# Performance work log

Measured on AMD Instinct MI355X. Metric: run time of the kernel, lower is better.

The kernel has to match this reference:

```python
import jax, jax.numpy as jnp
import numpy as np

T, B, A, H = 1024, 16, 8, 256


def setup_inputs() -> dict:
    key = jax.random.key(0)
    ks = jax.random.split(key, 8)
    s = 1.0 / np.sqrt(H)  # approximate lecun/orthogonal scale for stability
    return {
        "ins": jax.random.normal(ks[0], (T, B, A, H), dtype=jnp.float32),
        "resets": jax.random.randint(ks[1], (T, B, A), 0, 2) == 1,
        "h0": jnp.zeros((B, A, H), dtype=jnp.float32),
        "W_ir": jax.random.normal(ks[2], (H, H), dtype=jnp.float32) * s,
        "W_iz": jax.random.normal(ks[3], (H, H), dtype=jnp.float32) * s,
        "W_in": jax.random.normal(ks[4], (H, H), dtype=jnp.float32) * s,
        "b_ir": jnp.zeros((H,), dtype=jnp.float32),
        "b_iz": jnp.zeros((H,), dtype=jnp.float32),
        "b_in": jnp.zeros((H,), dtype=jnp.float32),
        "W_hr": jax.random.normal(ks[5], (H, H), dtype=jnp.float32) * s,
        "W_hz": jax.random.normal(ks[6], (H, H), dtype=jnp.float32) * s,
        "W_hn": jax.random.normal(ks[7], (H, H), dtype=jnp.float32) * s,
        "b_hn": jnp.zeros((H,), dtype=jnp.float32),
    }


def reference(ins, resets, h0, W_ir, W_iz, W_in, b_ir, b_iz, b_in, W_hr, W_hz, W_hn, b_hn):
    # Precompute the input-side gate projections for all timesteps at once
    # (mathematically identical to flax GRUCell's per-step dense_i calls).
    xr = ins @ W_ir + b_ir  # [T, B, A, H]
    xz = ins @ W_iz + b_iz
    xn = ins @ W_in + b_in

    def step(h, xs):
        xr_t, xz_t, xn_t, rst_t = xs
        # reset masking: re-init carry to zeros where episode resets
        h = jnp.where(rst_t[..., None], jnp.zeros_like(h), h)
        r = jax.nn.sigmoid(xr_t + h @ W_hr)
        z = jax.nn.sigmoid(xz_t + h @ W_hz)
        n = jnp.tanh(xn_t + r * (h @ W_hn + b_hn))
        new_h = (1.0 - z) * n + z * h
        return new_h, new_h

    final_h, ys = jax.lax.scan(step, h0, (xr, xz, xn, resets))
    return ys  # [T, B, A, H]; final carry == ys[-1]
```

## Files before the change

### kernel.cpp

```cpp
#include <hip/hip_runtime.h>

#define BA 128
#define H 256
#define TH 768
#define NROWS (1024 * BA)
#define LCAP 65536
#define NBUCK 8
#define MT 32
#define AP 264
#define NFRAG (8 * 48 * 64)

typedef _Float16 h2_t __attribute__((ext_vector_type(2)));
typedef _Float16 h8_t __attribute__((ext_vector_type(8)));
typedef short s8_t __attribute__((ext_vector_type(8)));
typedef float f4_t __attribute__((ext_vector_type(4)));
typedef unsigned short u16;
typedef u16 us4_t __attribute__((ext_vector_type(4)));
typedef unsigned int u32;
typedef u32 v64u __attribute__((ext_vector_type(64)));

__device__ __forceinline__ float bf2f(u16 u) {
  union { u32 i; float f; } c; c.i = ((u32)u) << 16; return c.f;
}
__device__ __forceinline__ u16 f2bf(float f) {
  union { float f; u32 i; } c; c.f = f;
  u32 r = c.i + 0x7FFFu + ((c.i >> 16) & 1u);
  return (u16)(r >> 16);
}
__device__ __forceinline__ float sigm(float x) {
  float e = __builtin_amdgcn_exp2f(-x * 1.442695040888963f);
  return __builtin_amdgcn_rcpf(1.0f + e);
}
__device__ __forceinline__ float tanh_(float x) {
  float e = __builtin_amdgcn_exp2f(x * 2.885390081777927f);
  return 1.0f - 2.0f * __builtin_amdgcn_rcpf(1.0f + e);
}
__device__ __forceinline__ float ldf(const void* p, bool f32, size_t idx) {
  return f32 ? ((const float*)p)[idx] : bf2f(((const u16*)p)[idx]);
}
__device__ __forceinline__ int ldrst(const void* p, bool isbyte, size_t idx) {
  return isbyte ? (int)((const unsigned char*)p)[idx] : ((const int*)p)[idx];
}
__device__ __forceinline__ float F2(h2_t a, h2_t b, float c) {
#if defined(__has_builtin) && __has_builtin(__builtin_amdgcn_fdot2)
  return __builtin_amdgcn_fdot2(a, b, c, false);
#else
  return c + (float)a[0] * (float)b[0] + (float)a[1] * (float)b[1];
#endif
}

__global__ __launch_bounds__(256) void kdetect(const u32* __restrict__ insw,
                                               const u32* __restrict__ rstw,
                                               const u32* __restrict__ whrw,
                                               const u32* __restrict__ wirw,
                                               int* __restrict__ flags,
                                               int* __restrict__ cnt) {
  __shared__ int c0, c1, c2, c3;
  if (threadIdx.x == 0) { c0 = 0; c1 = 0; c2 = 0; c3 = 0; }
  if (threadIdx.x < NBUCK) cnt[threadIdx.x] = 0;
  __syncthreads();
  if (!(fabsf(bf2f((u16)(insw[threadIdx.x] & 0xFFFFu))) < 1e10f)) atomicAdd(&c0, 1);
  if (!(fabsf(bf2f((u16)(whrw[threadIdx.x] & 0xFFFFu))) < 1e10f)) atomicAdd(&c2, 1);
  if (!(fabsf(bf2f((u16)(wirw[threadIdx.x] & 0xFFFFu))) < 1e10f)) atomicAdd(&c3, 1);
  if (threadIdx.x < 128 && rstw[threadIdx.x] > 1u) atomicAdd(&c1, 1);
  __syncthreads();
  if (threadIdx.x == 0) {
    flags[0] = (c0 > 8) ? 1 : 0;
    flags[1] = (c1 > 0) ? 1 : 0;
    flags[2] = (c2 > 8) ? 1 : 0;
    flags[3] = (c3 > 8) ? 1 : 0;
  }
}

__global__ __launch_bounds__(256) void ktrans(const void* __restrict__ W0, const void* __restrict__ W1,
                                              const void* __restrict__ W2, const void* __restrict__ W3,
                                              const void* __restrict__ W4, const void* __restrict__ W5,
                                              u16* __restrict__ WT, const int* __restrict__ flags) {
  __shared__ u16 tile[64][65];
  int g = blockIdx.z;
  bool f32in = ((g < 3) ? flags[3] : flags[2]) != 0;
  bool toF16 = (g >= 3);
  const void* srcs[6] = {W0, W1, W2, W3, W4, W5};
  const void* src = srcs[g];
  int k0 = blockIdx.x * 64, j0 = blockIdx.y * 64;
  int tid = threadIdx.x;
#pragma unroll
  for (int p = 0; p < 16; ++p) {
    int e = p * 256 + tid;
    int kr = e >> 6, jc = e & 63;
    size_t idx = (size_t)(k0 + kr) * H + j0 + jc;
    float v = f32in ? ((const float*)src)[idx] : bf2f(((const u16*)src)[idx]);
    u16 bits;
    if (toF16) {
      _Float16 h = (_Float16)v;
      bits = __builtin_bit_cast(u16, h);
    } else {
      bits = f2bf(v);
    }
    tile[kr][jc] = bits;
  }
  __syncthreads();
  u16* dst = WT + (size_t)g * H * H;
#pragma unroll
  for (int p = 0; p < 16; ++p) {
    int e = p * 256 + tid;
    int jr = e >> 6, kc = e & 63;
    dst[(size_t)(j0 + jr) * H + k0 + kc] = tile[kc][jr];
  }
}

__global__ __launch_bounds__(256) void kswz(const u16* __restrict__ WT, u16* __restrict__ WB) {
  int fl = blockIdx.x * 256 + threadIdx.x;
  if (fl >= NFRAG) return;
  int part = blockIdx.y;
  int lane = fl & 63;
  int cg = (fl >> 6) % 48;
  int kk = (fl >> 6) / 48;
  int g = part * 3 + (cg >> 4);
  int col = ((cg & 15) << 4) + (lane & 15);
  int k0 = kk * 32 + ((lane >> 4) << 3);
  const u16* src = WT + (size_t)g * H * H + (size_t)col * H + k0;
  *(s8_t*)(WB + ((size_t)part * NFRAG + fl) * 8) = *(const s8_t*)src;
}

__global__ __launch_bounds__(256) void kgemm(const void* __restrict__ ins,
                                             int t0, const u16* __restrict__ WiB,
                                             u16* __restrict__ C,
                                             const int* __restrict__ flags) {
  __shared__ __align__(16) u16 As[64 * AP];
  bool f32in = flags[0] != 0;
  int tid = threadIdx.x;
  int bt = blockIdx.x;
  int rh = blockIdx.y;
  size_t abase = ((size_t)(t0 + bt) * BA + rh * 64) * H;
#pragma unroll
  for (int q = 0; q < 8; ++q) {
    int idx = q * 256 + tid;
    int row = idx >> 5;
    int col0 = (idx & 31) * 8;
    s8_t v;
    if (f32in) {
      const float* s = (const float*)ins + abase + (size_t)idx * 8;
      f4_t x0 = *(const f4_t*)s;
      f4_t x1 = *(const f4_t*)(s + 4);
#pragma unroll
      for (int i = 0; i < 4; ++i) v[i] = (short)f2bf(x0[i]);
#pragma unroll
      for (int i = 0; i < 4; ++i) v[4 + i] = (short)f2bf(x1[i]);
    } else {
      v = *(const s8_t*)((const u16*)ins + abase + (size_t)idx * 8);
    }
    *(s8_t*)(As + row * AP + col0) = v;
  }
  __syncthreads();

  int lane = tid & 63;
  int wv = tid >> 6;
  int wr = wv >> 1;
  int wc = wv & 1;
  int r16 = lane & 15;
  int kg = lane >> 4;
  const s8_t* WB = (const s8_t*)WiB;
  int row0 = bt * 128 + rh * 64;

  for (int c = 0; c < 6; ++c) {
    f4_t acc[2][4];
#pragma unroll
    for (int a = 0; a < 2; ++a)
#pragma unroll
      for (int b = 0; b < 4; ++b) acc[a][b] = (f4_t)0.0f;
#pragma unroll 2
    for (int kk = 0; kk < 8; ++kk) {
      s8_t af[2];
#pragma unroll
      for (int mt = 0; mt < 2; ++mt)
        af[mt] = *(const s8_t*)(As + (wr * 32 + mt * 16 + r16) * AP + kk * 32 + kg * 8);
      s8_t bfr[4];
#pragma unroll
      for (int ct = 0; ct < 4; ++ct) {
        int cg = c * 8 + wc * 4 + ct;
        bfr[ct] = WB[(size_t)((kk * 48 + cg) * 64 + lane)];
      }
#pragma unroll
      for (int ct = 0; ct < 4; ++ct)
#pragma unroll
        for (int mt = 0; mt < 2; ++mt)
          acc[mt][ct] = __builtin_amdgcn_mfma_f32_16x16x32_bf16(af[mt], bfr[ct], acc[mt][ct], 0, 0, 0);
    }
#pragma unroll
    for (int mt = 0; mt < 2; ++mt)
#pragma unroll
      for (int ct = 0; ct < 4; ++ct)
#pragma unroll
        for (int r = 0; r < 4; ++r) {
          int grow = row0 + wr * 32 + mt * 16 + kg * 4 + r;
          int gcol = c * 128 + wc * 64 + ct * 16 + r16;
          C[(size_t)grow * TH + gcol] = f2bf(acc[mt][ct][r]);
        }
  }
}

__global__ __launch_bounds__(256) void kdlists(const void* __restrict__ resets,
                                               unsigned char* __restrict__ dbuf,
                                               int* __restrict__ cnt,
                                               u32* __restrict__ list,
                                               const int* __restrict__ flags) {
  bool rbyte = flags[1] != 0;
  int w = blockIdx.x;
  int tid = threadIdx.x;
  __shared__ unsigned char rst[1024];
  __shared__ unsigned char dS[1024];
  __shared__ int lcnt[NBUCK], lbase[NBUCK], lpos[NBUCK];
  if (tid < NBUCK) { lcnt[tid] = 0; lpos[tid] = 0; }
  for (int t = tid; t < 1024; t += 256)
    rst[t] = (unsigned char)(ldrst(resets, rbyte, (size_t)t * BA + w) != 0);
  __syncthreads();
#pragma unroll
  for (int p = 0; p < 4; ++p) {
    int t = p * 256 + tid;
    int d;
    if (rst[t]) {
      d = 255;
    } else {
      int tr = t - 1;
      while (tr >= 0 && !rst[tr]) --tr;
      d = t - ((tr >= 0) ? tr : 0);
      if (d > 254) d = 254;
    }
    dS[t] = (unsigned char)d;
    if (d < NBUCK) atomicAdd(&lcnt[d], 1);
  }
  __syncthreads();
  if (tid < NBUCK) lbase[tid] = atomicAdd(&cnt[tid], lcnt[tid]);
  for (int t = tid; t < 1024; t += 256) dbuf[(size_t)w * 1024 + t] = dS[t];
  __syncthreads();
#pragma unroll
  for (int p = 0; p < 4; ++p) {
    int t = p * 256 + tid;
    int d = dS[t];
    if (d < NBUCK) {
      int pos = lbase[d] + atomicAdd(&lpos[d], 1);
      if (pos < LCAP) list[(size_t)d * LCAP + pos] = (u32)(t * BA + w);
    }
  }
}

__global__ __launch_bounds__(256) void kelem(const u16* __restrict__ xproj,
                                             const void* __restrict__ resets,
                                             float* __restrict__ out,
                                             const void* __restrict__ bir, const void* __restrict__ biz,
                                             const void* __restrict__ bin_, const void* __restrict__ bhn,
                                             const int* __restrict__ flags) {
  bool rbyte = flags[1] != 0;
  bool wf32 = flags[2] != 0;
  int j = threadIdx.x;
  float vbir = ldf(bir, wf32, j), vbiz = ldf(biz, wf32, j);
  float vbin = ldf(bin_, wf32, j), vbhn = ldf(bhn, wf32, j);
  for (int i = blockIdx.x; i < NROWS; i += gridDim.x) {
    if (!ldrst(resets, rbyte, i)) continue;
    size_t xb = (size_t)i * TH + j;
    float r = sigm(bf2f(xproj[xb]) + vbir);
    float z = sigm(bf2f(xproj[xb + H]) + vbiz);
    float n = tanh_(bf2f(xproj[xb + 2 * H]) + vbin + r * vbhn);
    out[(size_t)i * H + j] = (1.0f - z) * n;
  }
}

__global__ __launch_bounds__(512) void kstep(const u16* __restrict__ xproj,
                                             float* __restrict__ out,
                                             const void* __restrict__ h0,
                                             const u16* __restrict__ WhB,
                                             const int* __restrict__ cnt,
                                             const u32* __restrict__ list,
                                             const void* __restrict__ bir, const void* __restrict__ biz,
                                             const void* __restrict__ bin_, const void* __restrict__ bhn,
                                             const int* __restrict__ flags, int s) {
  int cs = cnt[s];
  if (cs <= 0) return;
  bool wf32 = flags[2] != 0;
  __shared__ __align__(16) u16 As[MT * AP];
  __shared__ int ridS[MT];
  int tid = threadIdx.x;
  int lane = tid & 63;
  int wv = tid >> 6;
  int r16 = lane & 15;
  int kg = lane >> 4;
  int ntiles = (cs + MT - 1) / MT;
  float vb[2][4];
#pragma unroll
  for (int jt = 0; jt < 2; ++jt) {
    int j = wv * 32 + jt * 16 + r16;
    vb[jt][0] = ldf(bir, wf32, j);
    vb[jt][1] = ldf(biz, wf32, j);
    vb[jt][2] = ldf(bin_, wf32, j);
    vb[jt][3] = ldf(bhn, wf32, j);
  }
  const s8_t* WB = (const s8_t*)WhB;

  for (int tile = blockIdx.x; tile < ntiles; tile += gridDim.x) {
    __syncthreads();
    {
      int i = tid >> 4;
      int seg = tid & 15;
      int idx = tile * MT + i;
      int rid = (idx < cs) ? (int)list[idx] : -1;
      if (seg == 0) ridS[i] = rid;
      u16* dst = As + i * AP + seg * 16;
      if (rid >= 0) {
        if (s == 0) {
#pragma unroll
          for (int q = 0; q < 4; ++q) {
            us4_t hb;
#pragma unroll
            for (int e = 0; e < 4; ++e) {
              _Float16 hh = (_Float16)ldf(h0, wf32, (size_t)rid * H + seg * 16 + q * 4 + e);
              hb[e] = __builtin_bit_cast(u16, hh);
            }
            *(us4_t*)(dst + q * 4) = hb;
          }
        } else {
          const float* src = out + (size_t)(rid - BA) * H + seg * 16;
#pragma unroll
          for (int q = 0; q < 4; ++q) {
            f4_t v = *(const f4_t*)(src + q * 4);
            us4_t hb;
#pragma unroll
            for (int e = 0; e < 4; ++e) {
              _Float16 hh = (_Float16)v[e];
              hb[e] = __builtin_bit_cast(u16, hh);
            }
            *(us4_t*)(dst + q * 4) = hb;
          }
        }
      } else {
        us4_t hz; hz[0] = 0; hz[1] = 0; hz[2] = 0; hz[3] = 0;
#pragma unroll
        for (int q = 0; q < 4; ++q) *(us4_t*)(dst + q * 4) = hz;
      }
    }
    __syncthreads();

    f4_t acc[2][6];
#pragma unroll
    for (int a = 0; a < 2; ++a)
#pragma unroll
      for (int b = 0; b < 6; ++b) acc[a][b] = (f4_t)0.0f;

#pragma unroll 2
    for (int kk = 0; kk < 8; ++kk) {
      h8_t af[2];
#pragma unroll
      for (int mt = 0; mt < 2; ++mt)
        af[mt] = __builtin_bit_cast(h8_t,
            *(const s8_t*)(As + (mt * 16 + r16) * AP + kk * 32 + kg * 8));
      s8_t bfr[6];
#pragma unroll
      for (int g = 0; g < 3; ++g)
#pragma unroll
        for (int jt = 0; jt < 2; ++jt) {
          int cg = g * 16 + wv * 2 + jt;
          bfr[g * 2 + jt] = WB[(size_t)((kk * 48 + cg) * 64 + lane)];
        }
#pragma unroll
      for (int c = 0; c < 6; ++c)
#pragma unroll
        for (int mt = 0; mt < 2; ++mt)
          acc[mt][c] = __builtin_amdgcn_mfma_f32_16x16x32_f16(
              af[mt], __builtin_bit_cast(h8_t, bfr[c]), acc[mt][c], 0, 0, 0);
    }

#pragma unroll
    for (int mt = 0; mt < 2; ++mt)
#pragma unroll
      for (int r = 0; r < 4; ++r) {
        int rowl = mt * 16 + kg * 4 + r;
        int rid = ridS[rowl];
        if (rid < 0) continue;
#pragma unroll
        for (int jt = 0; jt < 2; ++jt) {
          int j = wv * 32 + jt * 16 + r16;
          size_t xb = (size_t)rid * TH + j;
          float rg = sigm(bf2f(xproj[xb]) + vb[jt][0] + acc[mt][jt][r]);
          float zg = sigm(bf2f(xproj[xb + H]) + vb[jt][1] + acc[mt][2 + jt][r]);
          float ng = tanh_(bf2f(xproj[xb + 2 * H]) + vb[jt][2] + rg * (acc[mt][4 + jt][r] + vb[jt][3]));
          float hp = (s == 0) ? ldf(h0, wf32, (size_t)rid * H + j)
                              : out[(size_t)(rid - BA) * H + j];
          out[(size_t)rid * H + j] = (1.0f - zg) * ng + zg * hp;
        }
      }
  }
}

#define LDW(VR, P, c) { uint4 q_ = *(const uint4*)((P) + (c) * 8); \
  VR[(c)*4+0] = q_.x; VR[(c)*4+1] = q_.y; VR[(c)*4+2] = q_.z; VR[(c)*4+3] = q_.w; }
#define LDWALL(VR, P) \
  LDW(VR,P,0) LDW(VR,P,1) LDW(VR,P,2) LDW(VR,P,3) LDW(VR,P,4) LDW(VR,P,5) LDW(VR,P,6) LDW(VR,P,7) \
  LDW(VR,P,8) LDW(VR,P,9) LDW(VR,P,10) LDW(VR,P,11) LDW(VR,P,12) LDW(VR,P,13) LDW(VR,P,14) LDW(VR,P,15)

#define BCH(x) __builtin_bit_cast(h2_t, (u32)(x))
#define DOTC(c) { uint4 hv_ = h4_[c]; \
  h2_t a0_ = __builtin_bit_cast(h2_t, hv_.x); \
  h2_t a1_ = __builtin_bit_cast(h2_t, hv_.y); \
  h2_t a2_ = __builtin_bit_cast(h2_t, hv_.z); \
  h2_t a3_ = __builtin_bit_cast(h2_t, hv_.w); \
  ar = F2(BCH(WR[4*(c)+0]), a0_, ar); az = F2(BCH(WZ[4*(c)+0]), a0_, az); an = F2(BCH(WN[4*(c)+0]), a0_, an); \
  ar = F2(BCH(WR[4*(c)+1]), a1_, ar); az = F2(BCH(WZ[4*(c)+1]), a1_, az); an = F2(BCH(WN[4*(c)+1]), a1_, an); \
  ar = F2(BCH(WR[4*(c)+2]), a2_, ar); az = F2(BCH(WZ[4*(c)+2]), a2_, az); an = F2(BCH(WN[4*(c)+2]), a2_, an); \
  ar = F2(BCH(WR[4*(c)+3]), a3_, ar); az = F2(BCH(WZ[4*(c)+3]), a3_, az); an = F2(BCH(WN[4*(c)+3]), a3_, an); }
#define DOT16 \
  DOTC(0) DOTC(1) DOTC(2) DOTC(3) DOTC(4) DOTC(5) DOTC(6) DOTC(7) \
  DOTC(8) DOTC(9) DOTC(10) DOTC(11) DOTC(12) DOTC(13) DOTC(14) DOTC(15)

__global__ __launch_bounds__(512, 2) void ktail(const u16* __restrict__ xproj,
                                                float* __restrict__ out,
                                                const u16* __restrict__ WhF,
                                                const unsigned char* __restrict__ dbuf,
                                                const void* __restrict__ bir, const void* __restrict__ biz,
                                                const void* __restrict__ bin_, const void* __restrict__ bhn,
                                                const int* __restrict__ flags) {
  int w = blockIdx.x;
  int tid = threadIdx.x;
  int j = tid >> 1;
  int half = tid & 1;
  bool wf32 = flags[2] != 0;
  __shared__ __align__(16) u16 hsb[256];
  __shared__ unsigned char dcol[1024];
  for (int t = tid; t < 1024; t += 512) dcol[t] = dbuf[(size_t)w * 1024 + t];
  const u16* pr = WhF + (size_t)j * H + half * 128;
  const u16* pz = WhF + (size_t)H * H + (size_t)j * H + half * 128;
  const u16* pn = WhF + (size_t)2 * H * H + (size_t)j * H + half * 128;
  v64u WR, WZ, WN;
  LDWALL(WR, pr)
  LDWALL(WZ, pz)
  LDWALL(WN, pn)
  float vbir = ldf(bir, wf32, j), vbiz = ldf(biz, wf32, j);
  float vbin = ldf(bin_, wf32, j), vbhn = ldf(bhn, wf32, j);
  __syncthreads();
  int prev_t = -99;
  float hreg = 0.0f;
#pragma unroll 1
  for (int t = 0; t < 1024; ++t) {
    int d = dcol[t];
    if (d < NBUCK || d == 255) continue;
    if (prev_t != t - 1) {
      hreg = out[((size_t)(t - 1) * BA + w) * H + j];
      if (half == 0) { _Float16 hh = (_Float16)hreg; hsb[j] = __builtin_bit_cast(u16, hh); }
      __syncthreads();
    }
    const uint4* h4_ = (const uint4*)(&hsb[half * 128]);
    float ar = 0.0f, az = 0.0f, an = 0.0f;
    DOT16
    ar += __shfl_xor(ar, 1, 64);
    az += __shfl_xor(az, 1, 64);
    an += __shfl_xor(an, 1, 64);
    size_t xb = ((size_t)t * BA + w) * TH + j;
    float r = sigm(bf2f(xproj[xb]) + vbir + ar);
    float z = sigm(bf2f(xproj[xb + H]) + vbiz + az);
    float n = tanh_(bf2f(xproj[xb + 2 * H]) + vbin + r * (an + vbhn));
    float hnew = (1.0f - z) * n + z * hreg;
    if (half == 0) out[((size_t)t * BA + w) * H + j] = hnew;
    __syncthreads();
    if (half == 0) { _Float16 hh = (_Float16)hnew; hsb[j] = __builtin_bit_cast(u16, hh); }
    hreg = hnew;
    prev_t = t;
    __syncthreads();
  }
}

__global__ __launch_bounds__(512, 2) void kscan(
    const u16* __restrict__ xproj, const void* __restrict__ resets,
    const void* __restrict__ h0, float* __restrict__ carry,
    const u16* __restrict__ WhF,
    const void* __restrict__ bir, const void* __restrict__ biz, const void* __restrict__ bin_,
    const void* __restrict__ bhn, float* __restrict__ out, int t0, int Tc,
    const int* __restrict__ flags) {
  int w = blockIdx.x;
  int tid = threadIdx.x;
  int j = tid >> 1;
  int half = tid & 1;
  bool wf32 = flags[2] != 0;
  bool rbyte = flags[1] != 0;
  __shared__ __align__(16) u16 hsb[2][256];
  __shared__ int rstS[1024];

  for (int t = tid; t < Tc; t += 512)
    rstS[t] = ldrst(resets, rbyte, (size_t)(t0 + t) * BA + w);

  const u16* pr = WhF + (size_t)j * H + half * 128;
  const u16* pz = WhF + (size_t)H * H + (size_t)j * H + half * 128;
  const u16* pn = WhF + (size_t)2 * H * H + (size_t)j * H + half * 128;
  v64u WR, WZ, WN;
  LDWALL(WR, pr)
  LDWALL(WZ, pz)
  LDWALL(WN, pn)

  float vbir = ldf(bir, wf32, j), vbiz = ldf(biz, wf32, j);
  float vbin = ldf(bin_, wf32, j), vbhn = ldf(bhn, wf32, j);

  float hreg = (t0 == 0) ? ldf(h0, wf32, (size_t)w * H + j) : carry[(size_t)w * H + j];
  __syncthreads();
  if (rstS[0] != 0) hreg = 0.0f;
  if (half == 0) {
    _Float16 hh = (_Float16)hreg;
    hsb[0][j] = __builtin_bit_cast(u16, hh);
  }
  __syncthreads();

  size_t xb0 = (size_t)w * TH + j;
  u16 cxr = xproj[xb0], cxz = xproj[xb0 + H], cxn = xproj[xb0 + 2 * H];

#pragma unroll 1
  for (int tl = 0; tl < Tc; ++tl) {
    u16 nxr = 0, nxz = 0, nxn = 0;
    if (tl + 1 < Tc) {
      size_t nb = ((size_t)(tl + 1) * BA + w) * TH + j;
      nxr = xproj[nb]; nxz = xproj[nb + H]; nxn = xproj[nb + 2 * H];
    }
    const uint4* h4_ = (const uint4*)(&hsb[tl & 1][half * 128]);
    float ar = 0.0f, az = 0.0f, an = 0.0f;
    DOT16
    ar += __shfl_xor(ar, 1, 64);
    az += __shfl_xor(az, 1, 64);
    an += __shfl_xor(an, 1, 64);
    float r = sigm(bf2f(cxr) + vbir + ar);
    float z = sigm(bf2f(cxz) + vbiz + az);
    float n = tanh_(bf2f(cxn) + vbin + r * (an + vbhn));
    float hnew = (1.0f - z) * n + z * hreg;
    if (half == 0) out[((size_t)(t0 + tl) * BA + w) * H + j] = hnew;

    float hnext = hnew;
    if (tl + 1 < Tc && rstS[tl + 1] != 0) hnext = 0.0f;
    if (half == 0) {
      _Float16 hh = (_Float16)hnext;
      hsb[(tl & 1) ^ 1][j] = __builtin_bit_cast(u16, hh);
    }
    hreg = hnext;
    cxr = nxr; cxz = nxz; cxn = nxn;
    __syncthreads();
  }
  if (half == 0) carry[(size_t)w * H + j] = hreg;
}

extern "C" void kernel_launch(void* const* d_in, const int* in_sizes, int n_in,
                              void* d_out, int out_size, void* d_ws, size_t ws_size,
                              hipStream_t stream) {
  const void* ins = d_in[0];
  const void* resets = d_in[1];
  const void* h0 = d_in[2];
  const void* Wir = d_in[3];
  const void* Wiz = d_in[4];
  const void* Win = d_in[5];
  const void* bir = d_in[6];
  const void* biz = d_in[7];
  const void* bin_ = d_in[8];
  const void* Whr = d_in[9];
  const void* Whz = d_in[10];
  const void* Whn = d_in[11];
  const void* bhn = d_in[12];
  float* out = (float*)d_out;

  const size_t off_wt = 256;
  const size_t wt_bytes = (size_t)6 * H * H * 2;
  const size_t off_carry = off_wt + wt_bytes;
  const size_t off_cnt = off_carry + (size_t)BA * H * 4;
  const size_t off_dbuf = off_cnt + 256;
  const size_t off_list = off_dbuf + NROWS;
  const size_t off_wb = off_list + (size_t)NBUCK * LCAP * 4;
  const size_t wb_bytes = (size_t)2 * TH * H * 2;
  const size_t off_xproj = off_wb + wb_bytes;
  const size_t chunk_bytes = (size_t)BA * TH * 2;

  int* flags = (int*)d_ws;
  u16* WT = (u16*)((char*)d_ws + off_wt);
  float* carry = (float*)((char*)d_ws + off_carry);
  int* cnt = (int*)((char*)d_ws + off_cnt);
  unsigned char* dbuf = (unsigned char*)((char*)d_ws + off_dbuf);
  u32* list = (u32*)((char*)d_ws + off_list);
  u16* WB = (u16*)((char*)d_ws + off_wb);
  u16* xproj = (u16*)((char*)d_ws + off_xproj);

  kdetect<<<1, 256, 0, stream>>>((const u32*)ins, (const u32*)resets,
                                 (const u32*)Whr, (const u32*)Wir, flags, cnt);
  ktrans<<<dim3(4, 4, 6), 256, 0, stream>>>(Wir, Wiz, Win, Whr, Whz, Whn, WT, flags);
  kswz<<<dim3(96, 2), 256, 0, stream>>>(WT, WB);

  const u16* WiB = WB;
  const u16* WhB = WB + (size_t)NFRAG * 8;
  const u16* WhT = WT + (size_t)3 * H * H;
  if (ws_size >= off_xproj + (size_t)1024 * chunk_bytes) {
    kdlists<<<128, 256, 0, stream>>>(resets, dbuf, cnt, list, flags);
    kgemm<<<dim3(1024, 2), 256, 0, stream>>>(ins, 0, WiB, xproj, flags);
    kelem<<<1024, 256, 0, stream>>>(xproj, resets, out, bir, biz, bin_, bhn, flags);
    for (int s = 0; s < NBUCK; ++s)
      kstep<<<1024, 512, 0, stream>>>(xproj, out, h0, WhB, cnt, list + (size_t)s * LCAP,
                                      bir, biz, bin_, bhn, flags, s);
    ktail<<<128, 512, 0, stream>>>(xproj, out, WhT, dbuf, bir, biz, bin_, bhn, flags);
  } else {
    int Tc = 1024;
    while (Tc > 1 && off_xproj + (size_t)Tc * chunk_bytes > ws_size) Tc >>= 1;
    int nchunks = 1024 / Tc;
    for (int c = 0; c < nchunks; ++c) {
      int t0 = c * Tc;
      kgemm<<<dim3(Tc, 2), 256, 0, stream>>>(ins, t0, WiB, xproj, flags);
      kscan<<<128, 512, 0, stream>>>(xproj, resets, h0, carry, WhT,
                                     bir, biz, bin_, bhn, out, t0, Tc, flags);
    }
  }
}
```

Before: 742.4 us.

## Fuse distance-list, reset-element and bucket step kernels into one cooperative kernel

Replaces the kdlists, kelem and eight kstep launches with a single cooperative kernel of 256 blocks. Grid-wide syncs separate the phases and the per-bucket steps, and each block strides over tiles instead of using a 1024-block grid. The goal is to remove launch overhead and the gaps between roughly ten small launches. The cost is lower parallelism per bucket and the overhead of grid barriers. If the cooperative launch fails, the code falls back to the old launch sequence.

Result: slower. 1.468 ms (+97.7%).

```diff
diff --git a/kernel.cpp b/kernel.cpp
--- a/kernel.cpp
+++ b/kernel.cpp
@@ -1,4 +1,5 @@
 #include <hip/hip_runtime.h>
+#include <hip/hip_cooperative_groups.h>
 
 #define BA 128
 #define H 256
@@ -9,6 +10,8 @@
 #define MT 32
 #define AP 264
 #define NFRAG (8 * 48 * 64)
+
+namespace cg = cooperative_groups;
 
 typedef _Float16 h2_t __attribute__((ext_vector_type(2)));
 typedef _Float16 h8_t __attribute__((ext_vector_type(8)));
@@ -197,6 +200,194 @@
           int gcol = c * 128 + wc * 64 + ct * 16 + r16;
           C[(size_t)grow * TH + gcol] = f2bf(acc[mt][ct][r]);
         }
+  }
+}
+
+__global__ __launch_bounds__(512) void kfused(
+    const u16* __restrict__ xproj, const void* __restrict__ resets,
+    const void* __restrict__ h0, const u16* __restrict__ WhB,
+    unsigned char* __restrict__ dbuf, int* __restrict__ cnt,
+    u32* __restrict__ list, float* __restrict__ out,
+    const void* __restrict__ bir, const void* __restrict__ biz,
+    const void* __restrict__ bin_, const void* __restrict__ bhn,
+    const int* __restrict__ flags) {
+  cg::grid_group gg = cg::this_grid();
+  __shared__ __align__(16) u16 As[MT * AP];
+  __shared__ int ridS[MT];
+  int tid = threadIdx.x;
+  int bid = blockIdx.x;
+  bool rbyte = flags[1] != 0;
+  bool wf32 = flags[2] != 0;
+
+  if (bid < 128) {
+    unsigned char* rstS = (unsigned char*)As;
+    unsigned char* dS = rstS + 1024;
+    int w = bid;
+    if (tid < NBUCK) { ridS[tid] = 0; ridS[16 + tid] = 0; }
+    for (int t = tid; t < 1024; t += 512)
+      rstS[t] = (unsigned char)(ldrst(resets, rbyte, (size_t)t * BA + w) != 0);
+    __syncthreads();
+#pragma unroll
+    for (int p = 0; p < 2; ++p) {
+      int t = p * 512 + tid;
+      int d;
+      if (rstS[t]) {
+        d = 255;
+      } else {
+        int tr = t - 1;
+        while (tr >= 0 && !rstS[tr]) --tr;
+        d = t - ((tr >= 0) ? tr : 0);
+        if (d > 254) d = 254;
+      }
+      dS[t] = (unsigned char)d;
+      if (d < NBUCK) atomicAdd(&ridS[d], 1);
+    }
+    __syncthreads();
+    if (tid < NBUCK) ridS[8 + tid] = atomicAdd(&cnt[tid], ridS[tid]);
+    for (int t = tid; t < 1024; t += 512) dbuf[(size_t)w * 1024 + t] = dS[t];
+    __syncthreads();
+#pragma unroll
+    for (int p = 0; p < 2; ++p) {
+      int t = p * 512 + tid;
+      int d = dS[t];
+      if (d < NBUCK) {
+        int pos = ridS[8 + d] + atomicAdd(&ridS[16 + d], 1);
+        if (pos < LCAP) list[(size_t)d * LCAP + pos] = (u32)(t * BA + w);
+      }
+    }
+  }
+  {
+    int j = tid & 255;
+    int rp = tid >> 8;
+    float vbir = ldf(bir, wf32, j), vbiz = ldf(biz, wf32, j);
+    float vbin = ldf(bin_, wf32, j), vbhn = ldf(bhn, wf32, j);
+    for (int i = bid * 2 + rp; i < NROWS; i += 512) {
+      if (!ldrst(resets, rbyte, i)) continue;
+      size_t xb = (size_t)i * TH + j;
+      float r = sigm(bf2f(xproj[xb]) + vbir);
+      float z = sigm(bf2f(xproj[xb + H]) + vbiz);
+      float n = tanh_(bf2f(xproj[xb + 2 * H]) + vbin + r * vbhn);
+      out[(size_t)i * H + j] = (1.0f - z) * n;
+    }
+  }
+  __threadfence();
+  gg.sync();
+
+  int lane = tid & 63;
+  int wv = tid >> 6;
+  int r16 = lane & 15;
+  int kg = lane >> 4;
+  float vb[2][4];
+#pragma unroll
+  for (int jt = 0; jt < 2; ++jt) {
+    int j = wv * 32 + jt * 16 + r16;
+    vb[jt][0] = ldf(bir, wf32, j);
+    vb[jt][1] = ldf(biz, wf32, j);
+    vb[jt][2] = ldf(bin_, wf32, j);
+    vb[jt][3] = ldf(bhn, wf32, j);
+  }
+  const s8_t* WB = (const s8_t*)WhB;
+
+  for (int s = 0; s < NBUCK; ++s) {
+    int cs = cnt[s];
+    const u32* lst = list + (size_t)s * LCAP;
+    if (cs > 0) {
+      int ntiles = (cs + MT - 1) / MT;
+      for (int tile = bid; tile < ntiles; tile += 256) {
+        __syncthreads();
+        {
+          int i = tid >> 4;
+          int seg = tid & 15;
+          int idx = tile * MT + i;
+          int rid = (idx < cs) ? (int)lst[idx] : -1;
+          if (seg == 0) ridS[i] = rid;
+          u16* dst = As + i * AP + seg * 16;
+          if (rid >= 0) {
+            if (s == 0) {
+#pragma unroll
+              for (int q = 0; q < 4; ++q) {
+                us4_t hb;
+#pragma unroll
+                for (int e = 0; e < 4; ++e) {
+                  _Float16 hh = (_Float16)ldf(h0, wf32, (size_t)rid * H + seg * 16 + q * 4 + e);
+                  hb[e] = __builtin_bit_cast(u16, hh);
+                }
+                *(us4_t*)(dst + q * 4) = hb;
+              }
+            } else {
+              const float* src = out + (size_t)(rid - BA) * H + seg * 16;
+#pragma unroll
+              for (int q = 0; q < 4; ++q) {
+                f4_t v = *(const f4_t*)(src + q * 4);
+                us4_t hb;
+#pragma unroll
+                for (int e = 0; e < 4; ++e) {
+                  _Float16 hh = (_Float16)v[e];
+                  hb[e] = __builtin_bit_cast(u16, hh);
+                }
+                *(us4_t*)(dst + q * 4) = hb;
+              }
+            }
+          } else {
+            us4_t hz; hz[0] = 0; hz[1] = 0; hz[2] = 0; hz[3] = 0;
+#pragma unroll
+            for (int q = 0; q < 4; ++q) *(us4_t*)(dst + q * 4) = hz;
+          }
+        }
+        __syncthreads();
+
+        f4_t acc[2][6];
+#pragma unroll
+        for (int a = 0; a < 2; ++a)
+#pragma unroll
+          for (int b = 0; b < 6; ++b) acc[a][b] = (f4_t)0.0f;
+
+#pragma unroll 2
+        for (int kk = 0; kk < 8; ++kk) {
+          h8_t af[2];
+#pragma unroll
+          for (int mt = 0; mt < 2; ++mt)
+            af[mt] = __builtin_bit_cast(h8_t,
+                *(const s8_t*)(As + (mt * 16 + r16) * AP + kk * 32 + kg * 8));
+          s8_t bfr[6];
+#pragma unroll
+          for (int g = 0; g < 3; ++g)
+#pragma unroll
+            for (int jt = 0; jt < 2; ++jt) {
+              int cgf = g * 16 + wv * 2 + jt;
+              bfr[g * 2 + jt] = WB[(size_t)((kk * 48 + cgf) * 64 + lane)];
+            }
+#pragma unroll
+          for (int c = 0; c < 6; ++c)
+#pragma unroll
+            for (int mt = 0; mt < 2; ++mt)
+              acc[mt][c] = __builtin_amdgcn_mfma_f32_16x16x32_f16(
+                  af[mt], __builtin_bit_cast(h8_t, bfr[c]), acc[mt][c], 0, 0, 0);
+        }
+
+#pragma unroll
+        for (int mt = 0; mt < 2; ++mt)
+#pragma unroll
+          for (int r = 0; r < 4; ++r) {
+            int rowl = mt * 16 + kg * 4 + r;
+            int rid = ridS[rowl];
+            if (rid < 0) continue;
+#pragma unroll
+            for (int jt = 0; jt < 2; ++jt) {
+              int j = wv * 32 + jt * 16 + r16;
+              size_t xb = (size_t)rid * TH + j;
+              float rg = sigm(bf2f(xproj[xb]) + vb[jt][0] + acc[mt][jt][r]);
+              float zg = sigm(bf2f(xproj[xb + H]) + vb[jt][1] + acc[mt][2 + jt][r]);
+              float ng = tanh_(bf2f(xproj[xb + 2 * H]) + vb[jt][2] + rg * (acc[mt][4 + jt][r] + vb[jt][3]));
+              float hp = (s == 0) ? ldf(h0, wf32, (size_t)rid * H + j)
+                                  : out[(size_t)(rid - BA) * H + j];
+              out[(size_t)rid * H + j] = (1.0f - zg) * ng + zg * hp;
+            }
+          }
+      }
+    }
+    __threadfence();
+    gg.sync();
   }
 }
 
@@ -358,8 +549,8 @@
       for (int g = 0; g < 3; ++g)
 #pragma unroll
         for (int jt = 0; jt < 2; ++jt) {
-          int cg = g * 16 + wv * 2 + jt;
-          bfr[g * 2 + jt] = WB[(size_t)((kk * 48 + cg) * 64 + lane)];
+          int cgf = g * 16 + wv * 2 + jt;
+          bfr[g * 2 + jt] = WB[(size_t)((kk * 48 + cgf) * 64 + lane)];
         }
 #pragma unroll
       for (int c = 0; c < 6; ++c)
@@ -588,12 +779,21 @@
   const u16* WhB = WB + (size_t)NFRAG * 8;
   const u16* WhT = WT + (size_t)3 * H * H;
   if (ws_size >= off_xproj + (size_t)1024 * chunk_bytes) {
-    kdlists<<<128, 256, 0, stream>>>(resets, dbuf, cnt, list, flags);
     kgemm<<<dim3(1024, 2), 256, 0, stream>>>(ins, 0, WiB, xproj, flags);
-    kelem<<<1024, 256, 0, stream>>>(xproj, resets, out, bir, biz, bin_, bhn, flags);
-    for (int s = 0; s < NBUCK; ++s)
-      kstep<<<1024, 512, 0, stream>>>(xproj, out, h0, WhB, cnt, list + (size_t)s * LCAP,
-                                      bir, biz, bin_, bhn, flags, s);
+    const u16* xp = xproj;
+    void* args[] = {(void*)&xp, (void*)&resets, (void*)&h0, (void*)&WhB,
+                    (void*)&dbuf, (void*)&cnt, (void*)&list, (void*)&out,
+                    (void*)&bir, (void*)&biz, (void*)&bin_, (void*)&bhn,
+                    (void*)&flags};
+    hipError_t ce = hipLaunchCooperativeKernel((const void*)kfused, dim3(256), dim3(512),
+                                               args, 0, stream);
+    if (ce != hipSuccess) {
+      kdlists<<<128, 256, 0, stream>>>(resets, dbuf, cnt, list, flags);
+      kelem<<<1024, 256, 0, stream>>>(xproj, resets, out, bir, biz, bin_, bhn, flags);
+      for (int s = 0; s < NBUCK; ++s)
+        kstep<<<1024, 512, 0, stream>>>(xproj, out, h0, WhB, cnt, list + (size_t)s * LCAP,
+                                        bir, biz, bin_, bhn, flags, s);
+    }
     ktail<<<128, 512, 0, stream>>>(xproj, out, WhT, dbuf, bir, biz, bin_, bhn, flags);
   } else {
     int Tc = 1024;
```
